# Kernel tuning notes

Measured on AMD Instinct MI355X. Metric: run time of the kernel, lower is better.

## Reference

```python
import jax, jax.numpy as jnp
import numpy as np

HID, HEADS, LAYERS, EDIM = 128, 2, 3, 1
HEAD_DIM = HID  # out_channels per head (concat=False -> mean over heads)
N_NODES, N_EDGES = 50000, 500000
LN_EPS = 1e-5


def _layer_norm(x, g, b):
    mu = x.mean(-1, keepdims=True)
    var = ((x - mu) ** 2).mean(-1, keepdims=True)
    return (x - mu) * jax.lax.rsqrt(var + LN_EPS) * g + b


def _transformer_conv(x, src, tgt, edge_attr, Wq, bq, Wk, bk, Wv, bv, We, Wskip, bskip):
    # PyG TransformerConv, concat=False, root_weight=True, lin_edge bias=False
    N = x.shape[0]
    E = src.shape[0]
    q = (x @ Wq + bq).reshape(N, HEADS, HEAD_DIM)
    k = (x @ Wk + bk).reshape(N, HEADS, HEAD_DIM)
    v = (x @ Wv + bv).reshape(N, HEADS, HEAD_DIM)
    e = (edge_attr @ We).reshape(E, HEADS, HEAD_DIM)          # [E,H,C]
    k_j = k[src] + e                                          # gather + edge bias
    q_i = q[tgt]
    alpha = (q_i * k_j).sum(-1) / jnp.sqrt(jnp.asarray(HEAD_DIM, x.dtype))  # [E,H]
    # scatter-softmax over incoming edges of each target node
    m = jax.ops.segment_max(alpha, tgt, num_segments=N)       # [N,H]
    a = jnp.exp(alpha - m[tgt])
    denom = jax.ops.segment_sum(a, tgt, num_segments=N)
    a = a / jnp.where(denom[tgt] > 0, denom[tgt], 1.0)
    msg = (v[src] + e) * a[..., None]                         # [E,H,C]
    out = jax.ops.segment_sum(msg, tgt, num_segments=N)       # [N,H,C]
    out = out.mean(axis=1)                                    # concat=False -> head mean
    return out + x @ Wskip + bskip                            # root/skip connection


def reference(x, edge_index, edge_attr, ln_in_g, ln_in_b,
              Wq, bq, Wk, bk, Wv, bv, We, Wskip, bskip, ln_g, ln_b):
    src, tgt = edge_index[0], edge_index[1]
    x = _layer_norm(x, ln_in_g, ln_in_b)
    for l in range(LAYERS):
        h = _transformer_conv(x, src, tgt, edge_attr,
                              Wq[l], bq[l], Wk[l], bk[l], Wv[l], bv[l],
                              We[l], Wskip[l], bskip[l])
        h = jax.nn.elu(h)
        x = _layer_norm(x + h, ln_g[l], ln_b[l])
    return x


def setup_inputs() -> dict:
    key = jax.random.key(0)
    ks = jax.random.split(key, 12)
    HC = HEADS * HEAD_DIM
    s = 1.0 / np.sqrt(HID)
    inp = {
        "x": jax.random.normal(ks[0], (N_NODES, HID), jnp.float32),
        "edge_index": jax.random.randint(ks[1], (2, N_EDGES), 0, N_NODES, jnp.int64),
        "edge_attr": jax.random.normal(ks[2], (N_EDGES, EDIM), jnp.float32),
        "ln_in_g": jnp.ones((HID,), jnp.float32),
        "ln_in_b": jnp.zeros((HID,), jnp.float32),
        "Wq": jax.random.normal(ks[3], (LAYERS, HID, HC), jnp.float32) * s,
        "bq": jnp.zeros((LAYERS, HC), jnp.float32),
        "Wk": jax.random.normal(ks[4], (LAYERS, HID, HC), jnp.float32) * s,
        "bk": jnp.zeros((LAYERS, HC), jnp.float32),
        "Wv": jax.random.normal(ks[5], (LAYERS, HID, HC), jnp.float32) * s,
        "bv": jnp.zeros((LAYERS, HC), jnp.float32),
        "We": jax.random.normal(ks[6], (LAYERS, EDIM, HC), jnp.float32),
        "Wskip": jax.random.normal(ks[7], (LAYERS, HID, HID), jnp.float32) * s,
        "bskip": jnp.zeros((LAYERS, HID), jnp.float32),
        "ln_g": jnp.ones((LAYERS, HID), jnp.float32),
        "ln_b": jnp.zeros((LAYERS, HID), jnp.float32),
    }
    return inp
```

## Files before the change

kernel.cpp:

```cpp
#include <hip/hip_runtime.h>
#include <math.h>

#define NN 50000
#define NE 500000
#define HIDS 128
#define MCOLS 896
#define NLAYERS 3

typedef __attribute__((ext_vector_type(8))) short short8;
typedef __attribute__((ext_vector_type(4))) float floatx4;
typedef _Float16 half8v __attribute__((ext_vector_type(8)));
typedef _Float16 half2v __attribute__((ext_vector_type(2)));

union H2U { half8v v; half2v h[4]; };

#define BSTR 152

#define LNB   12500
#define CNTB  1954
#define PKWB  1355
#define NCT   14
#define NBY   196
#define GEMM_BLOCKS (NCT * NBY)

static __device__ __forceinline__ unsigned short f2bf(float f) {
    unsigned u = __float_as_uint(f);
    u += 0x7fffu + ((u >> 16) & 1u);
    return (unsigned short)(u >> 16);
}
static __device__ __forceinline__ unsigned short f2h(float f) {
    union { _Float16 h; unsigned short u; } c;
    c.h = (_Float16)f;
    return c.u;
}
static __device__ __forceinline__ float fexp2(float x) {
    float r;
    asm("v_exp_f32 %0, %1" : "=v"(r) : "v"(x));
    return r;
}
#define DPP_ADD(v, ctrl) \
    v += __int_as_float(__builtin_amdgcn_mov_dpp(__float_as_int(v), ctrl, 0xf, 0xf, true))
static __device__ __forceinline__ float wred16(float v) {
    DPP_ADD(v, 0xB1);
    DPP_ADD(v, 0x4E);
    DPP_ADD(v, 0x124);
    DPP_ADD(v, 0x128);
    return v;
}
static __device__ __forceinline__ float wred64(float v) {
    v += __shfl_xor(v, 1, 64);
    v += __shfl_xor(v, 2, 64);
    v += __shfl_xor(v, 4, 64);
    v += __shfl_xor(v, 8, 64);
    v += __shfl_xor(v, 16, 64);
    v += __shfl_xor(v, 32, 64);
    return v;
}

__global__ __launch_bounds__(256) void eatb_fuseA(const float* __restrict__ x, const float* __restrict__ lg,
                                                  const float* __restrict__ lb, float* __restrict__ xout,
                                                  unsigned short* __restrict__ xb,
                                                  const int* __restrict__ tgt, int* __restrict__ cnt,
                                                  const float* __restrict__ Wq, const float* __restrict__ Wk,
                                                  const float* __restrict__ Wv, const float* __restrict__ Ws,
                                                  const float* __restrict__ bq, const float* __restrict__ bk,
                                                  const float* __restrict__ bv, const float* __restrict__ bs,
                                                  unsigned short* __restrict__ Wt, float* __restrict__ bcat) {
    int bid = blockIdx.x;
    if (bid < LNB) {
        int wid = threadIdx.x >> 6, lane = threadIdx.x & 63;
        int n = bid * 4 + wid;
        if (n >= NN) return;
        float2 v = *(const float2*)(x + (size_t)n * HIDS + 2 * lane);
        float mu = wred64(v.x + v.y) * (1.f / 128.f);
        float cx = v.x - mu, cy = v.y - mu;
        float var = wred64(cx * cx + cy * cy) * (1.f / 128.f);
        float r = rsqrtf(var + 1e-5f);
        float2 g2 = *(const float2*)(lg + 2 * lane);
        float2 b2 = *(const float2*)(lb + 2 * lane);
        float2 o;
        o.x = cx * r * g2.x + b2.x;
        o.y = cy * r * g2.y + b2.y;
        *(float2*)(xout + (size_t)n * HIDS + 2 * lane) = o;
        unsigned pk = (unsigned)f2bf(o.x) | ((unsigned)f2bf(o.y) << 16);
        *(unsigned*)(xb + (size_t)n * HIDS + 2 * lane) = pk;
    } else if (bid < LNB + CNTB) {
        int e = (bid - LNB) * 256 + threadIdx.x;
        if (e < NE) atomicAdd(&cnt[tgt[e]], 1);
    } else {
        const float QS = 0.08838834764831845f * 1.4426950408889634f;
        int idx = (bid - LNB - CNTB) * 256 + threadIdx.x;
        const int WTOT = NLAYERS * MCOLS * HIDS;
        if (idx < WTOT) {
            int l = idx / (MCOLS * HIDS);
            int rem = idx % (MCOLS * HIDS);
            int c = rem / HIDS, k = rem % HIDS;
            float v;
            if (c < 256)      v = Wq[(l * HIDS + k) * 256 + c] * QS;
            else if (c < 512) v = Wk[(l * HIDS + k) * 256 + c - 256];
            else if (c < 768) v = Wv[(l * HIDS + k) * 256 + c - 512];
            else              v = Ws[(l * HIDS + k) * 128 + c - 768];
            Wt[idx] = f2bf(v);
        } else {
            int i2 = idx - WTOT;
            if (i2 < NLAYERS * MCOLS) {
                int l = i2 / MCOLS, c = i2 % MCOLS;
                float v;
                if (c < 256)      v = bq[l * 256 + c] * QS;
                else if (c < 512) v = bk[l * 256 + c - 256];
                else if (c < 768) v = bv[l * 256 + c - 512];
                else              v = bs[l * 128 + c - 768];
                bcat[i2] = v;
            }
        }
    }
}

__global__ __launch_bounds__(256) void eatb_blocksum(const int* __restrict__ cnt, int* __restrict__ bsums) {
    __shared__ int sm[256];
    int i = blockIdx.x * 256 + threadIdx.x;
    sm[threadIdx.x] = (i < NN) ? cnt[i] : 0;
    __syncthreads();
    for (int off = 128; off > 0; off >>= 1) {
        if (threadIdx.x < off) sm[threadIdx.x] += sm[threadIdx.x + off];
        __syncthreads();
    }
    if (threadIdx.x == 0) bsums[blockIdx.x] = sm[0];
}

__global__ __launch_bounds__(256) void eatb_scanb(int* __restrict__ bsums, int nb) {
    __shared__ int sm[256];
    int t = threadIdx.x;
    int v = (t < nb) ? bsums[t] : 0;
    sm[t] = v;
    __syncthreads();
    for (int off = 1; off < 256; off <<= 1) {
        int x = (t >= off) ? sm[t - off] : 0;
        __syncthreads();
        sm[t] += x;
        __syncthreads();
    }
    if (t < nb) bsums[t] = sm[t] - v;
}

__global__ __launch_bounds__(256) void eatb_rowstart(const int* __restrict__ cnt, const int* __restrict__ bsums,
                                                     int* __restrict__ row_start) {
    __shared__ int sm[256];
    int t = threadIdx.x;
    int i = blockIdx.x * 256 + t;
    int v = (i < NN) ? cnt[i] : 0;
    sm[t] = v;
    __syncthreads();
    for (int off = 1; off < 256; off <<= 1) {
        int x = (t >= off) ? sm[t - off] : 0;
        __syncthreads();
        sm[t] += x;
        __syncthreads();
    }
    int excl = sm[t] - v + bsums[blockIdx.x];
    if (i < NN) row_start[i] = excl;
}

static __device__ __forceinline__ void gemm_body(int ct, int by,
                                                 const unsigned short* __restrict__ xb,
                                                 const unsigned short* __restrict__ Wt,
                                                 const float* __restrict__ bias,
                                                 unsigned short* __restrict__ qpack,
                                                 unsigned short* __restrict__ kvpack,
                                                 unsigned short* __restrict__ skipbuf,
                                                 short* Bs, unsigned short* Csh) {
    int tid = threadIdx.x;
    int wid = tid >> 6, lane = tid & 63;
    int fr = lane & 15;
    int kq = (lane >> 4) * 8;

    int brow = tid >> 4, bch = (tid & 15) * 8;
    #pragma unroll
    for (int p = 0; p < 4; ++p) {
        int r = brow + p * 16;
        *(uint4*)(Bs + r * BSTR + bch) = *(const uint4*)(Wt + (size_t)(ct * 64 + r) * HIDS + bch);
    }

    float bl[4];
    #pragma unroll
    for (int n = 0; n < 4; ++n) bl[n] = bias[ct * 64 + n * 16 + fr];

    unsigned short* dstb;
    int dstride, cbase;
    if (ct < 4)       { dstb = qpack;   dstride = 256; cbase = ct * 64; }
    else if (ct < 12) { dstb = kvpack;  dstride = 512; cbase = (ct - 4) * 64; }
    else              { dstb = skipbuf; dstride = 128; cbase = (ct - 12) * 64; }

    __syncthreads();

    int cl = (tid & 15) * 4;
    for (int s = 0; s < 4; ++s) {
        int r0 = by * 256 + s * 64;
        int ar = r0 + wid * 16 + fr;
        bool aok = ar < NN;
        const unsigned short* aptr = xb + (size_t)(aok ? ar : 0) * HIDS;

        floatx4 acc[4] = {};
        #pragma unroll
        for (int ks = 0; ks < 4; ++ks) {
            int kof = ks * 32 + kq;
            short8 af = *(const short8*)(aptr + kof);
            if (!aok) { short8 z = {}; af = z; }
            #pragma unroll
            for (int n = 0; n < 4; ++n) {
                short8 bf = *(const short8*)(Bs + (n * 16 + fr) * BSTR + kof);
                acc[n] = __builtin_amdgcn_mfma_f32_16x16x32_bf16(af, bf, acc[n], 0, 0, 0);
            }
        }
        unsigned short* Cb = Csh + (s & 1) * (64 * 68);
        #pragma unroll
        for (int n = 0; n < 4; ++n)
            #pragma unroll
            for (int rg = 0; rg < 4; ++rg)
                Cb[(wid * 16 + (lane >> 4) * 4 + rg) * 68 + n * 16 + fr] = f2h(acc[n][rg] + bl[n]);
        __syncthreads();
        #pragma unroll
        for (int p = 0; p < 4; ++p) {
            int rr = (tid >> 4) + 16 * p;
            int gr = r0 + rr;
            if (gr < NN) {
                ushort4 o = *(const ushort4*)(Cb + rr * 68 + cl);
                *(ushort4*)(dstb + (size_t)gr * dstride + cbase + cl) = o;
            }
        }
    }
}

__global__ __launch_bounds__(256) void eatb_gemm(const unsigned short* __restrict__ xb,
                                                 const unsigned short* __restrict__ Wt,
                                                 const float* __restrict__ bias,
                                                 unsigned short* __restrict__ qpack,
                                                 unsigned short* __restrict__ kvpack,
                                                 unsigned short* __restrict__ skipbuf) {
    __shared__ __align__(16) short Bs[64 * BSTR];
    __shared__ __align__(16) unsigned short Csh[2][64 * 68];
    gemm_body(blockIdx.x, blockIdx.y, xb, Wt, bias, qpack, kvpack, skipbuf, Bs, &Csh[0][0]);
}

__global__ __launch_bounds__(256) void eatb_fuseE(const unsigned short* __restrict__ xb,
                                                  const unsigned short* __restrict__ Wt,
                                                  const float* __restrict__ bias,
                                                  unsigned short* __restrict__ qpack,
                                                  unsigned short* __restrict__ kvpack,
                                                  unsigned short* __restrict__ skipbuf,
                                                  const int* __restrict__ src, const int* __restrict__ tgt,
                                                  const float* __restrict__ ea, int* __restrict__ row_state,
                                                  int2* __restrict__ csr) {
    __shared__ __align__(16) short Bs[64 * BSTR];
    __shared__ __align__(16) unsigned short Csh[2][64 * 68];
    int bid = blockIdx.x;
    if (bid < GEMM_BLOCKS) {
        gemm_body(bid / NBY, bid % NBY, xb, Wt, bias, qpack, kvpack, skipbuf, Bs, &Csh[0][0]);
    } else {
        int e = (bid - GEMM_BLOCKS) * 256 + threadIdx.x;
        if (e >= NE) return;
        int t = tgt[e];
        int pos = atomicAdd(&row_state[t], 1);
        int2 val;
        val.x = src[e];
        val.y = __float_as_int(ea[e]);
        csr[pos] = val;
    }
}

__global__ __launch_bounds__(256) void eatb_attn(const unsigned short* __restrict__ qpack,
                                                 const unsigned short* __restrict__ kvpack,
                                                 const unsigned short* __restrict__ skipbuf,
                                                 const int2* __restrict__ csr, const int* __restrict__ row_state,
                                                 const float* __restrict__ Wel, const float* __restrict__ g,
                                                 const float* __restrict__ beta, const float* __restrict__ xcur,
                                                 float* __restrict__ dst, unsigned short* __restrict__ xbout) {
    int wid = threadIdx.x >> 6;
    int lane = threadIdx.x & 63;
    int n = blockIdx.x * 4 + wid;
    if (n >= NN) return;
    int slot = lane >> 5;
    int h = (lane >> 4) & 1;
    int sl = lane & 15;
    int dbase = sl * 8;

    const _Float16* qh16 = (const _Float16*)qpack;
    const _Float16* kvh = (const _Float16*)kvpack;

    half8v qh = *(const half8v*)(qh16 + n * 256 + h * 128 + dbase);
    H2U qq; qq.v = qh;
    const float* wep = Wel + h * 128 + dbase;
    float qwe;
    {
        float4 wa = *(const float4*)wep;
        float4 wb = *(const float4*)(wep + 4);
        qwe = wred16((float)qh[0] * wa.x + (float)qh[1] * wa.y + (float)qh[2] * wa.z + (float)qh[3] * wa.w +
                     (float)qh[4] * wb.x + (float)qh[5] * wb.y + (float)qh[6] * wb.z + (float)qh[7] * wb.w);
    }

    float s0 = 0.f, s1 = 0.f, sea0 = 0.f, sea1 = 0.f;
    float a0[8] = {0.f, 0.f, 0.f, 0.f, 0.f, 0.f, 0.f, 0.f};
    float a1[8] = {0.f, 0.f, 0.f, 0.f, 0.f, 0.f, 0.f, 0.f};

    int end = row_state[n];
    int beg = (n > 0) ? row_state[n - 1] : 0;
    int nit = (end - beg + 7) >> 3;
    int lbase = (h << 7) + (sl << 3);

    int2 cA, cB, cC, cD;
    if (nit > 0) {
        int e = beg + slot;
        cA = csr[(e < end) ? e : beg];
        cB = csr[(e + 2 < end) ? e + 2 : beg];
        cC = csr[(e + 4 < end) ? e + 4 : beg];
        cD = csr[(e + 6 < end) ? e + 6 : beg];
    }

    for (int it = 0; it < nit; ++it) {
        int ebase = beg + 8 * it + slot;
        bool vA = ebase < end, vB = ebase + 2 < end, vC = ebase + 4 < end, vD = ebase + 6 < end;
        float eaA = __int_as_float(cA.y);
        float eaB = __int_as_float(cB.y);
        float eaC = __int_as_float(cC.y);
        float eaD = __int_as_float(cD.y);
        int koA = (cA.x << 9) + lbase;
        int koB = (cB.x << 9) + lbase;
        int koC = (cC.x << 9) + lbase;
        int koD = (cD.x << 9) + lbase;
        half8v kA = *(const half8v*)(kvh + koA);
        half8v kB = *(const half8v*)(kvh + koB);
        half8v kC = *(const half8v*)(kvh + koC);
        half8v kD = *(const half8v*)(kvh + koD);
        half8v vA8 = *(const half8v*)(kvh + koA + 256);
        half8v vB8 = *(const half8v*)(kvh + koB + 256);
        half8v vC8 = *(const half8v*)(kvh + koC + 256);
        half8v vD8 = *(const half8v*)(kvh + koD + 256);
        __builtin_amdgcn_sched_barrier(0);
        if (it + 1 < nit) {
            int e2 = ebase + 8;
            cA = csr[(e2 < end) ? e2 : beg];
            cB = csr[(e2 + 2 < end) ? e2 + 2 : beg];
            cC = csr[(e2 + 4 < end) ? e2 + 4 : beg];
            cD = csr[(e2 + 6 < end) ? e2 + 6 : beg];
        }

        H2U ka, kb, kc, kd;
        ka.v = kA; kb.v = kB; kc.v = kC; kd.v = kD;
        float dA0 = __builtin_amdgcn_fdot2(qq.h[0], ka.h[0], 0.f, false);
        float dA1 = __builtin_amdgcn_fdot2(qq.h[1], ka.h[1], 0.f, false);
        dA0 = __builtin_amdgcn_fdot2(qq.h[2], ka.h[2], dA0, false);
        dA1 = __builtin_amdgcn_fdot2(qq.h[3], ka.h[3], dA1, false);
        float dB0 = __builtin_amdgcn_fdot2(qq.h[0], kb.h[0], 0.f, false);
        float dB1 = __builtin_amdgcn_fdot2(qq.h[1], kb.h[1], 0.f, false);
        dB0 = __builtin_amdgcn_fdot2(qq.h[2], kb.h[2], dB0, false);
        dB1 = __builtin_amdgcn_fdot2(qq.h[3], kb.h[3], dB1, false);
        float dC0 = __builtin_amdgcn_fdot2(qq.h[0], kc.h[0], 0.f, false);
        float dC1 = __builtin_amdgcn_fdot2(qq.h[1], kc.h[1], 0.f, false);
        dC0 = __builtin_amdgcn_fdot2(qq.h[2], kc.h[2], dC0, false);
        dC1 = __builtin_amdgcn_fdot2(qq.h[3], kc.h[3], dC1, false);
        float dD0 = __builtin_amdgcn_fdot2(qq.h[0], kd.h[0], 0.f, false);
        float dD1 = __builtin_amdgcn_fdot2(qq.h[1], kd.h[1], 0.f, false);
        dD0 = __builtin_amdgcn_fdot2(qq.h[2], kd.h[2], dD0, false);
        dD1 = __builtin_amdgcn_fdot2(qq.h[3], kd.h[3], dD1, false);
        float pA = wred16(dA0 + dA1);
        float pB = wred16(dB0 + dB1);
        float pC = wred16(dC0 + dC1);
        float pD = wred16(dD0 + dD1);
        float wA = vA ? fexp2(fmaf(eaA, qwe, pA)) : 0.f;
        float wB = vB ? fexp2(fmaf(eaB, qwe, pB)) : 0.f;
        float wC = vC ? fexp2(fmaf(eaC, qwe, pC)) : 0.f;
        float wD = vD ? fexp2(fmaf(eaD, qwe, pD)) : 0.f;
        s0 += wA; s1 += wB; s0 += wC; s1 += wD;
        sea0 = fmaf(wA, eaA, sea0);
        sea1 = fmaf(wB, eaB, sea1);
        sea0 = fmaf(wC, eaC, sea0);
        sea1 = fmaf(wD, eaD, sea1);
        #pragma unroll
        for (int d = 0; d < 8; ++d) {
            a0[d] = fmaf(wA, (float)vA8[d], a0[d]);
            a1[d] = fmaf(wB, (float)vB8[d], a1[d]);
            a0[d] = fmaf(wC, (float)vC8[d], a0[d]);
            a1[d] = fmaf(wD, (float)vD8[d], a1[d]);
        }
    }

    float s = s0 + s1, sea = sea0 + sea1;
    float o0 = a0[0] + a1[0], o1 = a0[1] + a1[1], o2 = a0[2] + a1[2], o3 = a0[3] + a1[3];
    float o4 = a0[4] + a1[4], o5 = a0[5] + a1[5], o6 = a0[6] + a1[6], o7 = a0[7] + a1[7];

    s += __shfl_xor(s, 32, 64);
    sea += __shfl_xor(sea, 32, 64);
    o0 += __shfl_xor(o0, 32, 64);
    o1 += __shfl_xor(o1, 32, 64);
    o2 += __shfl_xor(o2, 32, 64);
    o3 += __shfl_xor(o3, 32, 64);
    o4 += __shfl_xor(o4, 32, 64);
    o5 += __shfl_xor(o5, 32, 64);
    o6 += __shfl_xor(o6, 32, 64);
    o7 += __shfl_xor(o7, 32, 64);

    float4 wea = *(const float4*)wep;
    float4 web = *(const float4*)(wep + 4);

    float inv = (s > 0.f) ? 1.f / s : 1.f;
    float sw = sea * inv;
    o0 = o0 * inv + sw * wea.x;
    o1 = o1 * inv + sw * wea.y;
    o2 = o2 * inv + sw * wea.z;
    o3 = o3 * inv + sw * wea.w;
    o4 = o4 * inv + sw * web.x;
    o5 = o5 * inv + sw * web.y;
    o6 = o6 * inv + sw * web.z;
    o7 = o7 * inv + sw * web.w;
    o0 = 0.5f * (o0 + __shfl_xor(o0, 16, 64));
    o1 = 0.5f * (o1 + __shfl_xor(o1, 16, 64));
    o2 = 0.5f * (o2 + __shfl_xor(o2, 16, 64));
    o3 = 0.5f * (o3 + __shfl_xor(o3, 16, 64));
    o4 = 0.5f * (o4 + __shfl_xor(o4, 16, 64));
    o5 = 0.5f * (o5 + __shfl_xor(o5, 16, 64));
    o6 = 0.5f * (o6 + __shfl_xor(o6, 16, 64));
    o7 = 0.5f * (o7 + __shfl_xor(o7, 16, 64));

    const _Float16* skp = (const _Float16*)skipbuf + n * 128 + dbase;
    half8v skh = *(const half8v*)skp;
    const float* xrp = xcur + n * 128 + dbase;
    float4 xra = *(const float4*)xrp, xrb = *(const float4*)(xrp + 4);
    float y0 = o0 + (float)skh[0], y1 = o1 + (float)skh[1], y2 = o2 + (float)skh[2], y3 = o3 + (float)skh[3];
    float y4 = o4 + (float)skh[4], y5 = o5 + (float)skh[5], y6 = o6 + (float)skh[6], y7 = o7 + (float)skh[7];
    y0 = (y0 > 0.f) ? y0 : __expf(y0) - 1.f;
    y1 = (y1 > 0.f) ? y1 : __expf(y1) - 1.f;
    y2 = (y2 > 0.f) ? y2 : __expf(y2) - 1.f;
    y3 = (y3 > 0.f) ? y3 : __expf(y3) - 1.f;
    y4 = (y4 > 0.f) ? y4 : __expf(y4) - 1.f;
    y5 = (y5 > 0.f) ? y5 : __expf(y5) - 1.f;
    y6 = (y6 > 0.f) ? y6 : __expf(y6) - 1.f;
    y7 = (y7 > 0.f) ? y7 : __expf(y7) - 1.f;
    float p0 = xra.x + y0, p1 = xra.y + y1, p2 = xra.z + y2, p3 = xra.w + y3;
    float p4 = xrb.x + y4, p5 = xrb.y + y5, p6 = xrb.z + y6, p7 = xrb.w + y7;
    float mu = wred16(p0 + p1 + p2 + p3 + p4 + p5 + p6 + p7) * (1.f / 128.f);
    float c0 = p0 - mu, c1 = p1 - mu, c2 = p2 - mu, c3 = p3 - mu;
    float c4 = p4 - mu, c5 = p5 - mu, c6 = p6 - mu, c7 = p7 - mu;
    float var = wred16(c0 * c0 + c1 * c1 + c2 * c2 + c3 * c3 +
                       c4 * c4 + c5 * c5 + c6 * c6 + c7 * c7) * (1.f / 128.f);
    float r = rsqrtf(var + 1e-5f);
    if (lane < 16) {
        const float* gp = g + dbase;
        const float* bp = beta + dbase;
        float4 ga = *(const float4*)gp, gb = *(const float4*)(gp + 4);
        float4 ba = *(const float4*)bp, bb = *(const float4*)(bp + 4);
        float4 oa, ob;
        oa.x = c0 * r * ga.x + ba.x; oa.y = c1 * r * ga.y + ba.y;
        oa.z = c2 * r * ga.z + ba.z; oa.w = c3 * r * ga.w + ba.w;
        ob.x = c4 * r * gb.x + bb.x; ob.y = c5 * r * gb.y + bb.y;
        ob.z = c6 * r * gb.z + bb.z; ob.w = c7 * r * gb.w + bb.w;
        float* dp = dst + n * 128 + dbase;
        *(float4*)dp = oa;
        *(float4*)(dp + 4) = ob;
        if (xbout) {
            uint4 pk;
            pk.x = (unsigned)f2bf(oa.x) | ((unsigned)f2bf(oa.y) << 16);
            pk.y = (unsigned)f2bf(oa.z) | ((unsigned)f2bf(oa.w) << 16);
            pk.z = (unsigned)f2bf(ob.x) | ((unsigned)f2bf(ob.y) << 16);
            pk.w = (unsigned)f2bf(ob.z) | ((unsigned)f2bf(ob.w) << 16);
            *(uint4*)(xbout + n * 128 + dbase) = pk;
        }
    }
}

extern "C" void kernel_launch(void* const* d_in, const int* in_sizes, int n_in,
                              void* d_out, int out_size, void* d_ws, size_t ws_size,
                              hipStream_t stream) {
    const float* x       = (const float*)d_in[0];
    const int*   ei      = (const int*)d_in[1];
    const float* eattr   = (const float*)d_in[2];
    const float* ln_in_g = (const float*)d_in[3];
    const float* ln_in_b = (const float*)d_in[4];
    const float* Wq = (const float*)d_in[5];
    const float* bq = (const float*)d_in[6];
    const float* Wk = (const float*)d_in[7];
    const float* bk = (const float*)d_in[8];
    const float* Wv = (const float*)d_in[9];
    const float* bv = (const float*)d_in[10];
    const float* We = (const float*)d_in[11];
    const float* Ws = (const float*)d_in[12];
    const float* bs = (const float*)d_in[13];
    const float* ln_g = (const float*)d_in[14];
    const float* ln_b = (const float*)d_in[15];
    float* out = (float*)d_out;

    char* p = (char*)d_ws;
    auto carve = [&](size_t bytes) {
        char* r = p;
        p += (bytes + 255) & ~(size_t)255;
        return (void*)r;
    };
    int*  cnt       = (int*)carve((size_t)NN * 4);
    int*  row_state = (int*)carve((size_t)NN * 4);
    int*  bsums     = (int*)carve(1024);
    int2* csr       = (int2*)carve((size_t)NE * 8);
    unsigned short* WcatT = (unsigned short*)carve((size_t)NLAYERS * MCOLS * HIDS * 2);
    float* bcat     = (float*)carve((size_t)NLAYERS * MCOLS * 4);
    float* xcur     = (float*)carve((size_t)NN * HIDS * 4);
    unsigned short* qpack  = (unsigned short*)carve((size_t)NN * 256 * 2);
    unsigned short* kvpack = (unsigned short*)carve((size_t)NN * 512 * 2);
    unsigned short* skipbuf = (unsigned short*)carve((size_t)NN * HIDS * 2);
    unsigned short* xb = (unsigned short*)carve((size_t)NN * HIDS * 2);

    const int NB_N = (NN + 255) / 256;
    const int NODE_BLOCKS = (NN + 3) / 4;

    hipMemsetAsync(cnt, 0, (size_t)NN * 4, stream);
    eatb_fuseA<<<LNB + CNTB + PKWB, 256, 0, stream>>>(x, ln_in_g, ln_in_b, xcur, xb,
                                                      ei + NE, cnt,
                                                      Wq, Wk, Wv, Ws, bq, bk, bv, bs, WcatT, bcat);

    eatb_blocksum<<<NB_N, 256, 0, stream>>>(cnt, bsums);
    eatb_scanb<<<1, 256, 0, stream>>>(bsums, NB_N);
    eatb_rowstart<<<NB_N, 256, 0, stream>>>(cnt, bsums, row_state);

    eatb_fuseE<<<GEMM_BLOCKS + CNTB, 256, 0, stream>>>(xb, WcatT, bcat, qpack, kvpack, skipbuf,
                                                       ei, ei + NE, eattr, row_state, csr);

    for (int l = 0; l < NLAYERS; ++l) {
        if (l > 0) {
            eatb_gemm<<<dim3(NCT, NBY), 256, 0, stream>>>(xb, WcatT + (size_t)l * MCOLS * HIDS,
                                                          bcat + (size_t)l * MCOLS, qpack, kvpack, skipbuf);
        }
        float* dst = (l == NLAYERS - 1) ? out : xcur;
        unsigned short* xbo = (l == NLAYERS - 1) ? nullptr : xb;
        eatb_attn<<<NODE_BLOCKS, 256, 0, stream>>>(qpack, kvpack, skipbuf, csr, row_state,
                                                   We + (size_t)l * 256, ln_g + (size_t)l * 128,
                                                   ln_b + (size_t)l * 128, xcur, dst, xbo);
    }
    (void)in_sizes; (void)n_in; (void)out_size; (void)ws_size;
}
```

Before: 504.9 us.

## Merge all stages into one persistent cooperative kernel with grid syncs

New measurement: 1.839 ms. 3.64x slower.

```diff
diff --git a/kernel.cpp b/kernel.cpp
--- a/kernel.cpp
+++ b/kernel.cpp
@@ -1,5 +1,8 @@
 #include <hip/hip_runtime.h>
+#include <hip/hip_cooperative_groups.h>
 #include <math.h>
+
+namespace cg = cooperative_groups;
 
 #define NN 50000
 #define NE 500000
@@ -22,6 +25,7 @@
 #define NCT   14
 #define NBY   196
 #define GEMM_BLOCKS (NCT * NBY)
+#define NB_N  196
 
 static __device__ __forceinline__ unsigned short f2bf(float f) {
     unsigned u = __float_as_uint(f);
@@ -57,79 +61,97 @@
     return v;
 }
 
-__global__ __launch_bounds__(256) void eatb_fuseA(const float* __restrict__ x, const float* __restrict__ lg,
-                                                  const float* __restrict__ lb, float* __restrict__ xout,
-                                                  unsigned short* __restrict__ xb,
-                                                  const int* __restrict__ tgt, int* __restrict__ cnt,
-                                                  const float* __restrict__ Wq, const float* __restrict__ Wk,
-                                                  const float* __restrict__ Wv, const float* __restrict__ Ws,
-                                                  const float* __restrict__ bq, const float* __restrict__ bk,
-                                                  const float* __restrict__ bv, const float* __restrict__ bs,
-                                                  unsigned short* __restrict__ Wt, float* __restrict__ bcat) {
-    int bid = blockIdx.x;
-    if (bid < LNB) {
+struct MonoP {
+    const float* x;
+    const int* src;
+    const int* tgt;
+    const float* eattr;
+    const float* ln_in_g;
+    const float* ln_in_b;
+    const float* Wq; const float* bq;
+    const float* Wk; const float* bk;
+    const float* Wv; const float* bv;
+    const float* We;
+    const float* Ws; const float* bs;
+    const float* ln_g; const float* ln_b;
+    float* out;
+    int* cnt;
+    int* row_state;
+    int* bsums;
+    int2* csr;
+    unsigned short* WcatT;
+    float* bcat;
+    float* xcur;
+    unsigned short* qpack;
+    unsigned short* kvpack;
+    unsigned short* skipbuf;
+    unsigned short* xb;
+};
+
+static __device__ __forceinline__ void fuseA_body(int vb, const MonoP& P) {
+    if (vb < LNB) {
         int wid = threadIdx.x >> 6, lane = threadIdx.x & 63;
-        int n = bid * 4 + wid;
-        if (n >= NN) return;
-        float2 v = *(const float2*)(x + (size_t)n * HIDS + 2 * lane);
-        float mu = wred64(v.x + v.y) * (1.f / 128.f);
-        float cx = v.x - mu, cy = v.y - mu;
-        float var = wred64(cx * cx + cy * cy) * (1.f / 128.f);
-        float r = rsqrtf(var + 1e-5f);
-        float2 g2 = *(const float2*)(lg + 2 * lane);
-        float2 b2 = *(const float2*)(lb + 2 * lane);
-        float2 o;
-        o.x = cx * r * g2.x + b2.x;
-        o.y = cy * r * g2.y + b2.y;
-        *(float2*)(xout + (size_t)n * HIDS + 2 * lane) = o;
-        unsigned pk = (unsigned)f2bf(o.x) | ((unsigned)f2bf(o.y) << 16);
-        *(unsigned*)(xb + (size_t)n * HIDS + 2 * lane) = pk;
-    } else if (bid < LNB + CNTB) {
-        int e = (bid - LNB) * 256 + threadIdx.x;
-        if (e < NE) atomicAdd(&cnt[tgt[e]], 1);
+        int n = vb * 4 + wid;
+        if (n < NN) {
+            float2 v = *(const float2*)(P.x + (size_t)n * HIDS + 2 * lane);
+            float mu = wred64(v.x + v.y) * (1.f / 128.f);
+            float cx = v.x - mu, cy = v.y - mu;
+            float var = wred64(cx * cx + cy * cy) * (1.f / 128.f);
+            float r = rsqrtf(var + 1e-5f);
+            float2 g2 = *(const float2*)(P.ln_in_g + 2 * lane);
+            float2 b2 = *(const float2*)(P.ln_in_b + 2 * lane);
+            float2 o;
+            o.x = cx * r * g2.x + b2.x;
+            o.y = cy * r * g2.y + b2.y;
+            *(float2*)(P.xcur + (size_t)n * HIDS + 2 * lane) = o;
+            unsigned pk = (unsigned)f2bf(o.x) | ((unsigned)f2bf(o.y) << 16);
+            *(unsigned*)(P.xb + (size_t)n * HIDS + 2 * lane) = pk;
+        }
+    } else if (vb < LNB + CNTB) {
+        int e = (vb - LNB) * 256 + threadIdx.x;
+        if (e < NE) atomicAdd(&P.cnt[P.tgt[e]], 1);
     } else {
         const float QS = 0.08838834764831845f * 1.4426950408889634f;
-        int idx = (bid - LNB - CNTB) * 256 + threadIdx.x;
+        int idx = (vb - LNB - CNTB) * 256 + threadIdx.x;
         const int WTOT = NLAYERS * MCOLS * HIDS;
         if (idx < WTOT) {
             int l = idx / (MCOLS * HIDS);
             int rem = idx % (MCOLS * HIDS);
             int c = rem / HIDS, k = rem % HIDS;
             float v;
-            if (c < 256)      v = Wq[(l * HIDS + k) * 256 + c] * QS;
-            else if (c < 512) v = Wk[(l * HIDS + k) * 256 + c - 256];
-            else if (c < 768) v = Wv[(l * HIDS + k) * 256 + c - 512];
-            else              v = Ws[(l * HIDS + k) * 128 + c - 768];
-            Wt[idx] = f2bf(v);
+            if (c < 256)      v = P.Wq[(l * HIDS + k) * 256 + c] * QS;
+            else if (c < 512) v = P.Wk[(l * HIDS + k) * 256 + c - 256];
+            else if (c < 768) v = P.Wv[(l * HIDS + k) * 256 + c - 512];
+            else              v = P.Ws[(l * HIDS + k) * 128 + c - 768];
+            P.WcatT[idx] = f2bf(v);
         } else {
             int i2 = idx - WTOT;
             if (i2 < NLAYERS * MCOLS) {
                 int l = i2 / MCOLS, c = i2 % MCOLS;
                 float v;
-                if (c < 256)      v = bq[l * 256 + c] * QS;
-                else if (c < 512) v = bk[l * 256 + c - 256];
-                else if (c < 768) v = bv[l * 256 + c - 512];
-                else              v = bs[l * 128 + c - 768];
-                bcat[i2] = v;
+                if (c < 256)      v = P.bq[l * 256 + c] * QS;
+                else if (c < 512) v = P.bk[l * 256 + c - 256];
+                else if (c < 768) v = P.bv[l * 256 + c - 512];
+                else              v = P.bs[l * 128 + c - 768];
+                P.bcat[i2] = v;
             }
         }
     }
 }
 
-__global__ __launch_bounds__(256) void eatb_blocksum(const int* __restrict__ cnt, int* __restrict__ bsums) {
-    __shared__ int sm[256];
-    int i = blockIdx.x * 256 + threadIdx.x;
+static __device__ __forceinline__ void blocksum_body(int vb, const int* cnt, int* bsums, int* sm) {
+    int i = vb * 256 + threadIdx.x;
     sm[threadIdx.x] = (i < NN) ? cnt[i] : 0;
     __syncthreads();
     for (int off = 128; off > 0; off >>= 1) {
         if (threadIdx.x < off) sm[threadIdx.x] += sm[threadIdx.x + off];
         __syncthreads();
     }
-    if (threadIdx.x == 0) bsums[blockIdx.x] = sm[0];
-}
-
-__global__ __launch_bounds__(256) void eatb_scanb(int* __restrict__ bsums, int nb) {
-    __shared__ int sm[256];
+    if (threadIdx.x == 0) bsums[vb] = sm[0];
+    __syncthreads();
+}
+
+static __device__ __forceinline__ void scanb_body(int* bsums, int nb, int* sm) {
     int t = threadIdx.x;
     int v = (t < nb) ? bsums[t] : 0;
     sm[t] = v;
@@ -141,13 +163,13 @@
         __syncthreads();
     }
     if (t < nb) bsums[t] = sm[t] - v;
-}
-
-__global__ __launch_bounds__(256) void eatb_rowstart(const int* __restrict__ cnt, const int* __restrict__ bsums,
-                                                     int* __restrict__ row_start) {
-    __shared__ int sm[256];
+    __syncthreads();
+}
+
+static __device__ __forceinline__ void rowstart_body(int vb, const int* cnt, const int* bsums,
+                                                     int* row_start, int* sm) {
     int t = threadIdx.x;
-    int i = blockIdx.x * 256 + t;
+    int i = vb * 256 + t;
     int v = (i < NN) ? cnt[i] : 0;
     sm[t] = v;
     __syncthreads();
@@ -157,8 +179,21 @@
         sm[t] += x;
         __syncthreads();
     }
-    int excl = sm[t] - v + bsums[blockIdx.x];
+    int excl = sm[t] - v + bsums[vb];
     if (i < NN) row_start[i] = excl;
+    __syncthreads();
+}
+
+static __device__ __forceinline__ void scatter_body(int vb, const MonoP& P) {
+    int e = vb * 256 + threadIdx.x;
+    if (e < NE) {
+        int t = P.tgt[e];
+        int pos = atomicAdd(&P.row_state[t], 1);
+        int2 val;
+        val.x = P.src[e];
+        val.y = __float_as_int(P.eattr[e]);
+        P.csr[pos] = val;
+    }
 }
 
 static __device__ __forceinline__ void gemm_body(int ct, int by,
@@ -229,63 +264,26 @@
             }
         }
     }
-}
-
-__global__ __launch_bounds__(256) void eatb_gemm(const unsigned short* __restrict__ xb,
-                                                 const unsigned short* __restrict__ Wt,
-                                                 const float* __restrict__ bias,
-                                                 unsigned short* __restrict__ qpack,
-                                                 unsigned short* __restrict__ kvpack,
-                                                 unsigned short* __restrict__ skipbuf) {
-    __shared__ __align__(16) short Bs[64 * BSTR];
-    __shared__ __align__(16) unsigned short Csh[2][64 * 68];
-    gemm_body(blockIdx.x, blockIdx.y, xb, Wt, bias, qpack, kvpack, skipbuf, Bs, &Csh[0][0]);
-}
-
-__global__ __launch_bounds__(256) void eatb_fuseE(const unsigned short* __restrict__ xb,
-                                                  const unsigned short* __restrict__ Wt,
-                                                  const float* __restrict__ bias,
-                                                  unsigned short* __restrict__ qpack,
-                                                  unsigned short* __restrict__ kvpack,
-                                                  unsigned short* __restrict__ skipbuf,
-                                                  const int* __restrict__ src, const int* __restrict__ tgt,
-                                                  const float* __restrict__ ea, int* __restrict__ row_state,
-                                                  int2* __restrict__ csr) {
-    __shared__ __align__(16) short Bs[64 * BSTR];
-    __shared__ __align__(16) unsigned short Csh[2][64 * 68];
-    int bid = blockIdx.x;
-    if (bid < GEMM_BLOCKS) {
-        gemm_body(bid / NBY, bid % NBY, xb, Wt, bias, qpack, kvpack, skipbuf, Bs, &Csh[0][0]);
-    } else {
-        int e = (bid - GEMM_BLOCKS) * 256 + threadIdx.x;
-        if (e >= NE) return;
-        int t = tgt[e];
-        int pos = atomicAdd(&row_state[t], 1);
-        int2 val;
-        val.x = src[e];
-        val.y = __float_as_int(ea[e]);
-        csr[pos] = val;
-    }
-}
-
-__global__ __launch_bounds__(256) void eatb_attn(const unsigned short* __restrict__ qpack,
-                                                 const unsigned short* __restrict__ kvpack,
-                                                 const unsigned short* __restrict__ skipbuf,
-                                                 const int2* __restrict__ csr, const int* __restrict__ row_state,
-                                                 const float* __restrict__ Wel, const float* __restrict__ g,
-                                                 const float* __restrict__ beta, const float* __restrict__ xcur,
-                                                 float* __restrict__ dst, unsigned short* __restrict__ xbout) {
+    __syncthreads();
+}
+
+static __device__ __forceinline__ void attn_body(int vb, const MonoP& P, int l,
+                                                 float* __restrict__ dst,
+                                                 unsigned short* __restrict__ xbout) {
     int wid = threadIdx.x >> 6;
     int lane = threadIdx.x & 63;
-    int n = blockIdx.x * 4 + wid;
+    int n = vb * 4 + wid;
     if (n >= NN) return;
     int slot = lane >> 5;
     int h = (lane >> 4) & 1;
     int sl = lane & 15;
     int dbase = sl * 8;
 
-    const _Float16* qh16 = (const _Float16*)qpack;
-    const _Float16* kvh = (const _Float16*)kvpack;
+    const _Float16* qh16 = (const _Float16*)P.qpack;
+    const _Float16* kvh = (const _Float16*)P.kvpack;
+    const float* Wel = P.We + (size_t)l * 256;
+    const float* g = P.ln_g + (size_t)l * 128;
+    const float* beta = P.ln_b + (size_t)l * 128;
 
     half8v qh = *(const half8v*)(qh16 + n * 256 + h * 128 + dbase);
     H2U qq; qq.v = qh;
@@ -302,10 +300,11 @@
     float a0[8] = {0.f, 0.f, 0.f, 0.f, 0.f, 0.f, 0.f, 0.f};
     float a1[8] = {0.f, 0.f, 0.f, 0.f, 0.f, 0.f, 0.f, 0.f};
 
-    int end = row_state[n];
-    int beg = (n > 0) ? row_state[n - 1] : 0;
+    int end = P.row_state[n];
+    int beg = (n > 0) ? P.row_state[n - 1] : 0;
     int nit = (end - beg + 7) >> 3;
     int lbase = (h << 7) + (sl << 3);
+    const int2* csr = P.csr;
 
     int2 cA, cB, cC, cD;
     if (nit > 0) {
@@ -421,9 +420,9 @@
     o6 = 0.5f * (o6 + __shfl_xor(o6, 16, 64));
     o7 = 0.5f * (o7 + __shfl_xor(o7, 16, 64));
 
-    const _Float16* skp = (const _Float16*)skipbuf + n * 128 + dbase;
+    const _Float16* skp = (const _Float16*)P.skipbuf + n * 128 + dbase;
     half8v skh = *(const half8v*)skp;
-    const float* xrp = xcur + n * 128 + dbase;
+    const float* xrp = P.xcur + n * 128 + dbase;
     float4 xra = *(const float4*)xrp, xrb = *(const float4*)(xrp + 4);
     float y0 = o0 + (float)skh[0], y1 = o1 + (float)skh[1], y2 = o2 + (float)skh[2], y3 = o3 + (float)skh[3];
     float y4 = o4 + (float)skh[4], y5 = o5 + (float)skh[5], y6 = o6 + (float)skh[6], y7 = o7 + (float)skh[7];
@@ -467,26 +466,73 @@
     }
 }
 
+__global__ __launch_bounds__(256, 4) void eatb_mono(MonoP P) {
+    cg::grid_group grid = cg::this_grid();
+    __shared__ __align__(16) short Bs[64 * BSTR];
+    __shared__ __align__(16) unsigned short Csh[2][64 * 68];
+    int* sm = (int*)Bs;
+    const int GB = gridDim.x;
+
+    for (int vb = blockIdx.x; vb < LNB + CNTB + PKWB; vb += GB)
+        fuseA_body(vb, P);
+    __threadfence(); grid.sync(); __threadfence();
+
+    for (int vb = blockIdx.x; vb < NB_N; vb += GB)
+        blocksum_body(vb, P.cnt, P.bsums, sm);
+    __threadfence(); grid.sync(); __threadfence();
+    if (blockIdx.x == 0) scanb_body(P.bsums, NB_N, sm);
+    __threadfence(); grid.sync(); __threadfence();
+    for (int vb = blockIdx.x; vb < NB_N; vb += GB)
+        rowstart_body(vb, P.cnt, P.bsums, P.row_state, sm);
+    __threadfence(); grid.sync(); __threadfence();
+
+    for (int vb = blockIdx.x; vb < GEMM_BLOCKS + CNTB; vb += GB) {
+        if (vb < GEMM_BLOCKS)
+            gemm_body(vb / NBY, vb % NBY, P.xb, P.WcatT, P.bcat,
+                      P.qpack, P.kvpack, P.skipbuf, Bs, &Csh[0][0]);
+        else
+            scatter_body(vb - GEMM_BLOCKS, P);
+    }
+    __threadfence(); grid.sync(); __threadfence();
+
+    for (int l = 0; l < NLAYERS; ++l) {
+        if (l > 0) {
+            for (int vb = blockIdx.x; vb < GEMM_BLOCKS; vb += GB)
+                gemm_body(vb / NBY, vb % NBY, P.xb, P.WcatT + (size_t)l * MCOLS * HIDS,
+                          P.bcat + (size_t)l * MCOLS, P.qpack, P.kvpack, P.skipbuf, Bs, &Csh[0][0]);
+            __threadfence(); grid.sync(); __threadfence();
+        }
+        float* dst = (l == NLAYERS - 1) ? P.out : P.xcur;
+        unsigned short* xbo = (l == NLAYERS - 1) ? nullptr : P.xb;
+        for (int vb = blockIdx.x; vb < LNB; vb += GB)
+            attn_body(vb, P, l, dst, xbo);
+        if (l < NLAYERS - 1) { __threadfence(); grid.sync(); __threadfence(); }
+    }
+}
+
 extern "C" void kernel_launch(void* const* d_in, const int* in_sizes, int n_in,
                               void* d_out, int out_size, void* d_ws, size_t ws_size,
                               hipStream_t stream) {
-    const float* x       = (const float*)d_in[0];
-    const int*   ei      = (const int*)d_in[1];
-    const float* eattr   = (const float*)d_in[2];
-    const float* ln_in_g = (const float*)d_in[3];
-    const float* ln_in_b = (const float*)d_in[4];
-    const float* Wq = (const float*)d_in[5];
-    const float* bq = (const float*)d_in[6];
-    const float* Wk = (const float*)d_in[7];
-    const float* bk = (const float*)d_in[8];
-    const float* Wv = (const float*)d_in[9];
-    const float* bv = (const float*)d_in[10];
-    const float* We = (const float*)d_in[11];
-    const float* Ws = (const float*)d_in[12];
-    const float* bs = (const float*)d_in[13];
-    const float* ln_g = (const float*)d_in[14];
-    const float* ln_b = (const float*)d_in[15];
-    float* out = (float*)d_out;
+    MonoP P;
+    P.x       = (const float*)d_in[0];
+    const int* ei = (const int*)d_in[1];
+    P.src     = ei;
+    P.tgt     = ei + NE;
+    P.eattr   = (const float*)d_in[2];
+    P.ln_in_g = (const float*)d_in[3];
+    P.ln_in_b = (const float*)d_in[4];
+    P.Wq = (const float*)d_in[5];
+    P.bq = (const float*)d_in[6];
+    P.Wk = (const float*)d_in[7];
+    P.bk = (const float*)d_in[8];
+    P.Wv = (const float*)d_in[9];
+    P.bv = (const float*)d_in[10];
+    P.We = (const float*)d_in[11];
+    P.Ws = (const float*)d_in[12];
+    P.bs = (const float*)d_in[13];
+    P.ln_g = (const float*)d_in[14];
+    P.ln_b = (const float*)d_in[15];
+    P.out = (float*)d_out;
 
     char* p = (char*)d_ws;
     auto carve = [&](size_t bytes) {
@@ -494,43 +540,28 @@
         p += (bytes + 255) & ~(size_t)255;
         return (void*)r;
     };
-    int*  cnt       = (int*)carve((size_t)NN * 4);
-    int*  row_state = (int*)carve((size_t)NN * 4);
-    int*  bsums     = (int*)carve(1024);
-    int2* csr       = (int2*)carve((size_t)NE * 8);
-    unsigned short* WcatT = (unsigned short*)carve((size_t)NLAYERS * MCOLS * HIDS * 2);
-    float* bcat     = (float*)carve((size_t)NLAYERS * MCOLS * 4);
-    float* xcur     = (float*)carve((size_t)NN * HIDS * 4);
-    unsigned short* qpack  = (unsigned short*)carve((size_t)NN * 256 * 2);
-    unsigned short* kvpack = (unsigned short*)carve((size_t)NN * 512 * 2);
-    unsigned short* skipbuf = (unsigned short*)carve((size_t)NN * HIDS * 2);
-    unsigned short* xb = (unsigned short*)carve((size_t)NN * HIDS * 2);
-
-    const int NB_N = (NN + 255) / 256;
-    const int NODE_BLOCKS = (NN + 3) / 4;
-
-    hipMemsetAsync(cnt, 0, (size_t)NN * 4, stream);
-    eatb_fuseA<<<LNB + CNTB + PKWB, 256, 0, stream>>>(x, ln_in_g, ln_in_b, xcur, xb,
-                                                      ei + NE, cnt,
-                                                      Wq, Wk, Wv, Ws, bq, bk, bv, bs, WcatT, bcat);
-
-    eatb_blocksum<<<NB_N, 256, 0, stream>>>(cnt, bsums);
-    eatb_scanb<<<1, 256, 0, stream>>>(bsums, NB_N);
-    eatb_rowstart<<<NB_N, 256, 0, stream>>>(cnt, bsums, row_state);
-
-    eatb_fuseE<<<GEMM_BLOCKS + CNTB, 256, 0, stream>>>(xb, WcatT, bcat, qpack, kvpack, skipbuf,
-                                                       ei, ei + NE, eattr, row_state, csr);
-
-    for (int l = 0; l < NLAYERS; ++l) {
-        if (l > 0) {
-            eatb_gemm<<<dim3(NCT, NBY), 256, 0, stream>>>(xb, WcatT + (size_t)l * MCOLS * HIDS,
-                                                          bcat + (size_t)l * MCOLS, qpack, kvpack, skipbuf);
-        }
-        float* dst = (l == NLAYERS - 1) ? out : xcur;
-        unsigned short* xbo = (l == NLAYERS - 1) ? nullptr : xb;
-        eatb_attn<<<NODE_BLOCKS, 256, 0, stream>>>(qpack, kvpack, skipbuf, csr, row_state,
-                                                   We + (size_t)l * 256, ln_g + (size_t)l * 128,
-                                                   ln_b + (size_t)l * 128, xcur, dst, xbo);
-    }
+    P.cnt       = (int*)carve((size_t)NN * 4);
+    P.row_state = (int*)carve((size_t)NN * 4);
+    P.bsums     = (int*)carve(1024);
+    P.csr       = (int2*)carve((size_t)NE * 8);
+    P.WcatT     = (unsigned short*)carve((size_t)NLAYERS * MCOLS * HIDS * 2);
+    P.bcat      = (float*)carve((size_t)NLAYERS * MCOLS * 4);
+    P.xcur      = (float*)carve((size_t)NN * HIDS * 4);
+    P.qpack     = (unsigned short*)carve((size_t)NN * 256 * 2);
+    P.kvpack    = (unsigned short*)carve((size_t)NN * 512 * 2);
+    P.skipbuf   = (unsigned short*)carve((size_t)NN * HIDS * 2);
+    P.xb        = (unsigned short*)carve((size_t)NN * HIDS * 2);
+
+    hipMemsetAsync(P.cnt, 0, (size_t)NN * 4, stream);
+
+    int maxB = 0;
+    hipOccupancyMaxActiveBlocksPerMultiprocessor(&maxB, eatb_mono, 256, 0);
+    if (maxB < 1) maxB = 1;
+    if (maxB > 4) maxB = 4;
+    int grid = maxB * 256;
+
+    void* kargs[] = { (void*)&P };
+    hipLaunchCooperativeKernel((void*)eatb_mono, dim3(grid), dim3(256), kargs, 0, stream);
+
     (void)in_sizes; (void)n_in; (void)out_size; (void)ws_size;
 }
```
